# Optimization experiments

Measured on AMD Instinct MI355X. Metric: run time of the kernel, lower is better.

The kernel has to match this reference:

```python
import jax, jax.numpy as jnp
import numpy as np

N_HEADS = 8
N_GROUPS = 32
EPS = 1e-6


def setup_inputs() -> dict:
    key = jax.random.key(0)
    ks = jax.random.split(key, 8)
    b, c, n, K = 2, 512, 1024, 64
    x = jax.random.normal(ks[0], (b, c, n), dtype=jnp.float32)
    valid_mask = jax.random.randint(ks[1], (n, K), 0, 2, dtype=jnp.int32)
    # ensure every query attends to at least one key (avoids all--inf softmax rows)
    valid_mask = valid_mask.at[:, 0].set(1)
    attend_idx = jax.random.randint(ks[2], (n, K), 0, n, dtype=jnp.int64)
    scale = 0.03
    return {
        "x": x,
        "valid_mask": valid_mask,
        "attend_idx": attend_idx,
        "gn_gamma": jnp.ones((c,), jnp.float32),
        "gn_beta": jnp.zeros((c,), jnp.float32),
        "wq": jax.random.normal(ks[3], (c, c), jnp.float32) * scale,
        "bq": jnp.zeros((c,), jnp.float32),
        "wk": jax.random.normal(ks[4], (c, c), jnp.float32) * scale,
        "bk": jnp.zeros((c,), jnp.float32),
        "wv": jax.random.normal(ks[5], (c, c), jnp.float32) * scale,
        "bv": jnp.zeros((c,), jnp.float32),
        "wo": jax.random.normal(ks[6], (c, c), jnp.float32) * scale,
        "bo": jnp.zeros((c,), jnp.float32),
    }


def _group_norm(x, gamma, beta):
    b, c, n = x.shape
    xr = x.reshape(b, N_GROUPS, c // N_GROUPS, n)
    mu = xr.mean(axis=(2, 3), keepdims=True)
    var = xr.var(axis=(2, 3), keepdims=True)
    h = ((xr - mu) * jax.lax.rsqrt(var + EPS)).reshape(b, c, n)
    return h * gamma[None, :, None] + beta[None, :, None]


def reference(x, valid_mask, attend_idx, gn_gamma, gn_beta,
              wq, bq, wk, bk, wv, bv, wo, bo):
    b, c, n = x.shape
    H = N_HEADS
    dh = c // H
    h = _group_norm(x, gn_gamma, gn_beta)
    # 1x1 Conv1d == per-node linear projection
    proj = lambda w, bias: jnp.einsum('oc,bcn->bon', w, h) + bias[None, :, None]
    q = proj(wq, bq).reshape(b, H, dh, n)
    k = proj(wk, bk).reshape(b, H, dh, n)
    v = proj(wv, bv).reshape(b, H, dh, n)
    # gather attendable keys/values per query: [b, H, nq, K, dh]
    kT = jnp.transpose(k, (0, 1, 3, 2))  # [b, H, n, dh]
    vT = jnp.transpose(v, (0, 1, 3, 2))
    keys = jnp.take(kT, attend_idx, axis=2)
    vals = jnp.take(vT, attend_idx, axis=2)
    # NOTE: sparse_forward uses beta=1 (no 1/sqrt(dh) scaling)
    w = jnp.einsum('bhqkc,bhcq->bhqk', keys, q)
    w = jnp.where(valid_mask[None, None] == 0, -jnp.inf, w)
    w = jax.nn.softmax(w, axis=-1)
    o = jnp.einsum('bhqk,bhqkc->bhqc', w, vals)  # [b, H, n, dh]
    # permute(0,3,1,2).reshape(b,c,n): channel layout is (dh, H)
    o = jnp.transpose(o, (0, 3, 1, 2)).reshape(b, c, n)
    out = x + jnp.einsum('oc,bcn->bon', wo, o) + bo[None, :, None]
    return out
```

## Files before the change

### kernel.cpp

```cpp
#include <hip/hip_runtime.h>
#include <hip/hip_bf16.h>

#define B_   2
#define C_   512
#define N_   1024
#define KK_  64
#define H_   8
#define DH_  64
#define NG_  32
#define MQKV 1536

typedef __attribute__((ext_vector_type(8))) short short8;
typedef __attribute__((ext_vector_type(4))) float f32x4;

__device__ __forceinline__ float ldf(const void* p, size_t i, int isbf) {
  return isbf ? __bfloat162float(((const __hip_bfloat16*)p)[i])
              : ((const float*)p)[i];
}
__device__ __forceinline__ unsigned short f2bfu(float f) {
  __hip_bfloat16 h = __float2bfloat16(f);
  unsigned short u; __builtin_memcpy(&u, &h, 2); return u;
}
__device__ __forceinline__ float bfu2f(unsigned short u) {
  return __uint_as_float(((unsigned)u) << 16);
}
__device__ __forceinline__ int detect_bf(const void* gamma) {
  return ((const unsigned*)gamma)[0] == 0x3F803F80u;
}

__global__ __launch_bounds__(256) void conv_k(
    const void* x, const void* wq, const void* wk, const void* wv, const void* wo,
    const void* bq, const void* bk, const void* bv, const void* bo,
    const void* gamma, unsigned short* __restrict__ wqkv,
    unsigned short* __restrict__ wob, float* __restrict__ bqkv,
    float* __restrict__ bof, float2* __restrict__ part) {
  const int isbf = detect_bf(gamma);
  const int tid = threadIdx.x;
  int idx = blockIdx.x * 256 + tid;
  if (idx < MQKV * C_) {
    int m = idx >> 9, c = idx & 511;
    const void* src = (m < 512) ? wq : (m < 1024 ? wk : wv);
    wqkv[idx] = f2bfu(ldf(src, (size_t)(m & 511) * C_ + c, isbf));
  }
  if (idx < C_ * C_) wob[idx] = f2bfu(ldf(wo, idx, isbf));
  if (idx < MQKV) {
    const void* src = (idx < 512) ? bq : (idx < 1024 ? bk : bv);
    bqkv[idx] = ldf(src, idx & 511, isbf);
  }
  if (idx < C_) bof[idx] = ldf(bo, idx, isbf);

  __shared__ float ssum[256], ssq[256];
  if (blockIdx.x < 256) {
    const size_t base = (size_t)blockIdx.x * 4096;
    float sum = 0.f, sq = 0.f;
    if (isbf) {
      const uint4* p = (const uint4*)((const unsigned short*)x + base);
      for (int t = tid; t < 512; t += 256) {
        uint4 u = p[t];
        unsigned wv4[4] = {u.x, u.y, u.z, u.w};
#pragma unroll
        for (int q = 0; q < 4; q++) {
          float a = __uint_as_float(wv4[q] << 16);
          float b = __uint_as_float(wv4[q] & 0xffff0000u);
          sum += a + b; sq += a * a + b * b;
        }
      }
    } else {
      const float4* p = (const float4*)((const float*)x + base);
      for (int t = tid; t < 1024; t += 256) {
        float4 v = p[t];
        sum += v.x + v.y + v.z + v.w;
        sq  += v.x * v.x + v.y * v.y + v.z * v.z + v.w * v.w;
      }
    }
    ssum[tid] = sum; ssq[tid] = sq;
    __syncthreads();
    for (int s = 128; s > 0; s >>= 1) {
      if (tid < s) { ssum[tid] += ssum[tid + s]; ssq[tid] += ssq[tid + s]; }
      __syncthreads();
    }
    if (tid == 0) part[blockIdx.x] = make_float2(ssum[0], ssq[0]);
  }
}

__global__ __launch_bounds__(256) void gn_apply_k(
    const void* x, const void* gamma, const void* beta,
    const float2* __restrict__ part, unsigned short* __restrict__ hT) {
  const int isbf = detect_bf(gamma);
  const int n0 = blockIdx.x * 64, c0 = blockIdx.y * 64, b = blockIdx.z;
  const int tid = threadIdx.x;
  __shared__ unsigned short Lt[64][72];
#pragma unroll
  for (int p = 0; p < 2; p++) {
    int idx = tid + p * 256;
    int cl = idx >> 3, seg = idx & 7;
    int c = c0 + cl;
    int bgi = (b * NG_ + (c >> 4)) * 4;
    float2 p0 = part[bgi], p1 = part[bgi + 1], p2 = part[bgi + 2], p3 = part[bgi + 3];
    float S = p0.x + p1.x + p2.x + p3.x;
    float Q = p0.y + p1.y + p2.y + p3.y;
    float mu = S * (1.f / 16384.f);
    float rs = rsqrtf(fmaxf(Q * (1.f / 16384.f) - mu * mu, 0.f) + 1e-6f);
    float ga = ldf(gamma, c, isbf), be = ldf(beta, c, isbf);
    size_t srow = ((size_t)b * C_ + c) * N_ + n0 + seg * 8;
    float v[8];
    if (isbf) {
      uint4 u = *(const uint4*)((const unsigned short*)x + srow);
      v[0] = __uint_as_float(u.x << 16); v[1] = __uint_as_float(u.x & 0xffff0000u);
      v[2] = __uint_as_float(u.y << 16); v[3] = __uint_as_float(u.y & 0xffff0000u);
      v[4] = __uint_as_float(u.z << 16); v[5] = __uint_as_float(u.z & 0xffff0000u);
      v[6] = __uint_as_float(u.w << 16); v[7] = __uint_as_float(u.w & 0xffff0000u);
    } else {
      float4 a = *(const float4*)((const float*)x + srow);
      float4 bb = *(const float4*)((const float*)x + srow + 4);
      v[0] = a.x; v[1] = a.y; v[2] = a.z; v[3] = a.w;
      v[4] = bb.x; v[5] = bb.y; v[6] = bb.z; v[7] = bb.w;
    }
#pragma unroll
    for (int e = 0; e < 8; e++)
      Lt[seg * 8 + e][cl] = f2bfu((v[e] - mu) * rs * ga + be);
  }
  __syncthreads();
#pragma unroll
  for (int p = 0; p < 2; p++) {
    int idx = tid + p * 256;
    int nl = idx >> 3, seg = idx & 7;
    uint4 v = *(const uint4*)&Lt[nl][seg * 8];
    *(uint4*)&hT[((size_t)b * N_ + n0 + nl) * C_ + c0 + seg * 8] = v;
  }
}

__global__ __launch_bounds__(256) void qkv_gemm_k(
    const unsigned short* __restrict__ wqkv, const unsigned short* __restrict__ hT,
    const float* __restrict__ bqkv, unsigned short* __restrict__ qkv) {
  __shared__ short As[4096], Bs[4096];
  const int tid = threadIdx.x;
  const int lane = tid & 63, wave = tid >> 6;
  const int wm = wave >> 1, wn = wave & 1;
  const int n0 = blockIdx.x * 128;
  const int m0 = blockIdx.y * 128;
  const int b  = blockIdx.z;
  const unsigned short* Bbase = hT + (size_t)b * N_ * C_;

  f32x4 acc[4][4];
#pragma unroll
  for (int i = 0; i < 4; i++)
#pragma unroll
    for (int j = 0; j < 4; j++) acc[i][j] = (f32x4){0.f, 0.f, 0.f, 0.f};

  for (int k0 = 0; k0 < C_; k0 += 32) {
    __syncthreads();
#pragma unroll
    for (int p = 0; p < 2; p++) {
      int i = tid + p * 256;
      int sub = i >> 6, l = i & 63;
      int r = l & 15, kh = (l >> 4) << 3;
      *(uint4*)&As[i * 8] =
          *(const uint4*)&wqkv[(size_t)(m0 + sub * 16 + r) * C_ + k0 + kh];
      *(uint4*)&Bs[i * 8] =
          *(const uint4*)&Bbase[(size_t)(n0 + sub * 16 + r) * C_ + k0 + kh];
    }
    __syncthreads();
    const short8* Av = (const short8*)As;
    const short8* Bv = (const short8*)Bs;
    short8 af[4], bg[4];
#pragma unroll
    for (int i = 0; i < 4; i++) af[i] = Av[(wm * 4 + i) * 64 + lane];
#pragma unroll
    for (int j = 0; j < 4; j++) bg[j] = Bv[(wn * 4 + j) * 64 + lane];
#pragma unroll
    for (int i = 0; i < 4; i++)
#pragma unroll
      for (int j = 0; j < 4; j++)
        acc[i][j] = __builtin_amdgcn_mfma_f32_16x16x32_bf16(af[i], bg[j], acc[i][j], 0, 0, 0);
  }

  const int mb = m0 + wm * 64;
#pragma unroll
  for (int i = 0; i < 4; i++) {
    int mrow0 = mb + i * 16 + ((lane >> 4) << 2);
    int mat = mrow0 >> 9, head = (mrow0 >> 6) & 7, d0 = mrow0 & 63;
    float b0 = bqkv[mrow0], b1 = bqkv[mrow0 + 1], b2 = bqkv[mrow0 + 2], b3 = bqkv[mrow0 + 3];
#pragma unroll
    for (int j = 0; j < 4; j++) {
      int n = n0 + wn * 64 + j * 16 + (lane & 15);
      uint2 st;
      st.x = (unsigned)f2bfu(acc[i][j][0] + b0) | ((unsigned)f2bfu(acc[i][j][1] + b1) << 16);
      st.y = (unsigned)f2bfu(acc[i][j][2] + b2) | ((unsigned)f2bfu(acc[i][j][3] + b3) << 16);
      size_t dst = (size_t)mat * ((size_t)B_ * H_ * N_ * DH_) +
                   (((size_t)b * H_ + head) * N_ + n) * DH_ + d0;
      *(uint2*)&qkv[dst] = st;
    }
  }
}

__global__ __launch_bounds__(512) void attn_k(
    const unsigned short* __restrict__ qkv, const void* aidx,
    const int* __restrict__ vmask, unsigned short* __restrict__ ocT) {
  const int tid = threadIdx.x, w = tid >> 6, lane = tid & 63;
  const int b = blockIdx.x >> 10, qi = blockIdx.x & 1023;

  const unsigned* aw = (const unsigned*)aidx;
  unsigned long long bal = __ballot(aw[2 * lane + 1] != 0u);
  const int is64 = (bal == 0ull);

  __shared__ float qs[8][64];
  __shared__ float wl[8][64];
  __shared__ int   il[8][64];
  __shared__ unsigned short olds[512];

  const size_t S = (size_t)B_ * H_ * N_ * DH_;
  const unsigned short* qT = qkv;
  const unsigned short* kT = qkv + S;
  const unsigned short* vT = qkv + 2 * S;
  const size_t bh = ((size_t)b * H_ + w) * N_;

  qs[w][lane] = bfu2f(qT[(bh + qi) * DH_ + lane]);
  const size_t ai = (size_t)qi * KK_ + lane;
  int idx = is64 ? (int)((const long long*)aidx)[ai] : ((const int*)aidx)[ai];
  idx &= (N_ - 1);
  const int valid = vmask[ai];
  __threadfence_block();

  const uint4* k4 = (const uint4*)&kT[(bh + idx) * DH_];
  float s = 0.f;
#pragma unroll
  for (int j2 = 0; j2 < 8; j2++) {
    uint4 u = k4[j2];
    const float* q8 = &qs[w][j2 * 8];
    s += __uint_as_float(u.x << 16) * q8[0] + __uint_as_float(u.x & 0xffff0000u) * q8[1]
       + __uint_as_float(u.y << 16) * q8[2] + __uint_as_float(u.y & 0xffff0000u) * q8[3]
       + __uint_as_float(u.z << 16) * q8[4] + __uint_as_float(u.z & 0xffff0000u) * q8[5]
       + __uint_as_float(u.w << 16) * q8[6] + __uint_as_float(u.w & 0xffff0000u) * q8[7];
  }
  s = valid ? s : -INFINITY;

  float m = s;
#pragma unroll
  for (int off = 32; off > 0; off >>= 1) m = fmaxf(m, __shfl_xor(m, off));
  float e = valid ? __expf(s - m) : 0.f;
  float sum = e;
#pragma unroll
  for (int off = 32; off > 0; off >>= 1) sum += __shfl_xor(sum, off);

  wl[w][lane] = (sum > 0.f) ? (e / sum) : 0.f;
  il[w][lane] = idx;
  __threadfence_block();

  const unsigned short* vbase = vT + bh * DH_;
  float acc = 0.f;
#pragma unroll 16
  for (int ki = 0; ki < KK_; ki++)
    acc += wl[w][ki] * bfu2f(vbase[(size_t)il[w][ki] * DH_ + lane]);

  olds[lane * H_ + w] = f2bfu(acc);
  __syncthreads();
  if (tid < 64) {
    uint4 vv = *(const uint4*)&olds[tid * 8];
    *(uint4*)&ocT[((size_t)b * N_ + qi) * C_ + tid * 8] = vv;
  }
}

__global__ __launch_bounds__(256) void out_gemm_k(
    const unsigned short* __restrict__ wob, const unsigned short* __restrict__ ocT,
    const float* __restrict__ bof, const void* __restrict__ x,
    const void* gamma, void* __restrict__ out) {
  const int isbf = detect_bf(gamma);
  __shared__ short As[4096], Bs[4096];
  const int tid = threadIdx.x;
  const int lane = tid & 63, wave = tid >> 6;
  const int wm = wave >> 1, wn = wave & 1;
  const int n0 = blockIdx.x * 128;
  const int m0 = blockIdx.y * 128;
  const int b  = blockIdx.z;
  const unsigned short* Bbase = ocT + (size_t)b * N_ * C_;

  f32x4 acc[4][4];
#pragma unroll
  for (int i = 0; i < 4; i++)
#pragma unroll
    for (int j = 0; j < 4; j++) acc[i][j] = (f32x4){0.f, 0.f, 0.f, 0.f};

  for (int k0 = 0; k0 < C_; k0 += 32) {
    __syncthreads();
#pragma unroll
    for (int p = 0; p < 2; p++) {
      int i = tid + p * 256;
      int sub = i >> 6, l = i & 63;
      int r = l & 15, kh = (l >> 4) << 3;
      *(uint4*)&As[i * 8] =
          *(const uint4*)&wob[(size_t)(m0 + sub * 16 + r) * C_ + k0 + kh];
      *(uint4*)&Bs[i * 8] =
          *(const uint4*)&Bbase[(size_t)(n0 + sub * 16 + r) * C_ + k0 + kh];
    }
    __syncthreads();
    const short8* Av = (const short8*)As;
    const short8* Bv = (const short8*)Bs;
    short8 af[4], bg[4];
#pragma unroll
    for (int i = 0; i < 4; i++) af[i] = Av[(wm * 4 + i) * 64 + lane];
#pragma unroll
    for (int j = 0; j < 4; j++) bg[j] = Bv[(wn * 4 + j) * 64 + lane];
#pragma unroll
    for (int i = 0; i < 4; i++)
#pragma unroll
      for (int j = 0; j < 4; j++)
        acc[i][j] = __builtin_amdgcn_mfma_f32_16x16x32_bf16(bg[j], af[i], acc[i][j], 0, 0, 0);
  }

#pragma unroll
  for (int i = 0; i < 4; i++) {
    int m = m0 + wm * 64 + i * 16 + (lane & 15);
    float bias = bof[m];
#pragma unroll
    for (int j = 0; j < 4; j++) {
      int nb = n0 + wn * 64 + j * 16 + ((lane >> 4) << 2);
      size_t oi = ((size_t)b * C_ + m) * N_ + nb;
      if (isbf) {
        const unsigned short* xp = (const unsigned short*)x;
        uint2 xv = *(const uint2*)&xp[oi];
        uint2 st;
        st.x = (unsigned)f2bfu(bfu2f((unsigned short)(xv.x & 0xffff)) + acc[i][j][0] + bias) |
               ((unsigned)f2bfu(bfu2f((unsigned short)(xv.x >> 16)) + acc[i][j][1] + bias) << 16);
        st.y = (unsigned)f2bfu(bfu2f((unsigned short)(xv.y & 0xffff)) + acc[i][j][2] + bias) |
               ((unsigned)f2bfu(bfu2f((unsigned short)(xv.y >> 16)) + acc[i][j][3] + bias) << 16);
        *(uint2*)&((unsigned short*)out)[oi] = st;
      } else {
        const float* xp = (const float*)x;
        float4 xv = *(const float4*)&xp[oi];
        float4 st;
        st.x = xv.x + acc[i][j][0] + bias;
        st.y = xv.y + acc[i][j][1] + bias;
        st.z = xv.z + acc[i][j][2] + bias;
        st.w = xv.w + acc[i][j][3] + bias;
        *(float4*)&((float*)out)[oi] = st;
      }
    }
  }
}

extern "C" void kernel_launch(void* const* d_in, const int* in_sizes, int n_in,
                              void* d_out, int out_size, void* d_ws, size_t ws_size,
                              hipStream_t stream) {
  const void* x     = d_in[0];
  const int*  vmask = (const int*)d_in[1];
  const void* aidx  = d_in[2];
  const void* gamma = d_in[3];
  const void* beta  = d_in[4];
  const void* wq = d_in[5],  *bq = d_in[6];
  const void* wk = d_in[7],  *bk = d_in[8];
  const void* wv = d_in[9],  *bv = d_in[10];
  const void* wo = d_in[11], *bo = d_in[12];

  char* wsb = (char*)d_ws;
  float2* part = (float2*)wsb;
  float*  bqkv = (float*)(wsb + 4096);
  float*  bof  = (float*)(wsb + 12288);
  unsigned short* wqkv = (unsigned short*)(wsb + 16384);
  unsigned short* wob  = wqkv + (size_t)MQKV * C_;
  unsigned short* hT   = wob + (size_t)C_ * C_;
  unsigned short* qkv  = hT + (size_t)B_ * N_ * C_;
  unsigned short* ocT  = qkv + (size_t)3 * B_ * H_ * N_ * DH_;

  conv_k<<<(MQKV * C_) / 256, 256, 0, stream>>>(x, wq, wk, wv, wo, bq, bk, bv, bo,
                                                gamma, wqkv, wob, bqkv, bof, part);
  gn_apply_k<<<dim3(N_ / 64, C_ / 64, B_), 256, 0, stream>>>(x, gamma, beta, part, hT);
  qkv_gemm_k<<<dim3(N_ / 128, MQKV / 128, B_), 256, 0, stream>>>(wqkv, hT, bqkv, qkv);
  attn_k<<<B_ * N_, 512, 0, stream>>>(qkv, aidx, vmask, ocT);
  out_gemm_k<<<dim3(N_ / 128, C_ / 128, B_), 256, 0, stream>>>(wob, ocT, bof, x, gamma, d_out);
}
```

Measured before the change: 156.1 us.

## Fuse weight conversion and group-norm apply into GEMM loads with double buffering

Drops the separate weight-conversion and group-norm-apply kernels. The GEMMs now read fp32 weights and raw x directly, converting to bf16 on the fly and applying a precomputed per-channel scale and shift from a small finalize kernel. Both GEMMs gain register prefetch with double-buffered shared memory so global loads overlap the MFMA work. The cost is that weights are converted redundantly in every block, and the x loads in the QKV GEMM become strided scalar reads along the channel axis, which are less coalesced.

```diff
diff --git a/kernel.cpp b/kernel.cpp
--- a/kernel.cpp
+++ b/kernel.cpp
@@ -8,7 +8,6 @@
 #define H_   8
 #define DH_  64
 #define NG_  32
-#define MQKV 1536
 
 typedef __attribute__((ext_vector_type(8))) short short8;
 typedef __attribute__((ext_vector_type(4))) float f32x4;
@@ -28,119 +27,106 @@
   return ((const unsigned*)gamma)[0] == 0x3F803F80u;
 }
 
-__global__ __launch_bounds__(256) void conv_k(
-    const void* x, const void* wq, const void* wk, const void* wv, const void* wo,
-    const void* bq, const void* bk, const void* bv, const void* bo,
-    const void* gamma, unsigned short* __restrict__ wqkv,
-    unsigned short* __restrict__ wob, float* __restrict__ bqkv,
-    float* __restrict__ bof, float2* __restrict__ part) {
+__global__ __launch_bounds__(256) void stats_k(
+    const void* x, const void* gamma, float2* __restrict__ part) {
   const int isbf = detect_bf(gamma);
   const int tid = threadIdx.x;
-  int idx = blockIdx.x * 256 + tid;
-  if (idx < MQKV * C_) {
-    int m = idx >> 9, c = idx & 511;
-    const void* src = (m < 512) ? wq : (m < 1024 ? wk : wv);
-    wqkv[idx] = f2bfu(ldf(src, (size_t)(m & 511) * C_ + c, isbf));
-  }
-  if (idx < C_ * C_) wob[idx] = f2bfu(ldf(wo, idx, isbf));
-  if (idx < MQKV) {
-    const void* src = (idx < 512) ? bq : (idx < 1024 ? bk : bv);
-    bqkv[idx] = ldf(src, idx & 511, isbf);
-  }
-  if (idx < C_) bof[idx] = ldf(bo, idx, isbf);
-
+  const size_t base = (size_t)blockIdx.x * 4096;
   __shared__ float ssum[256], ssq[256];
-  if (blockIdx.x < 256) {
-    const size_t base = (size_t)blockIdx.x * 4096;
-    float sum = 0.f, sq = 0.f;
-    if (isbf) {
-      const uint4* p = (const uint4*)((const unsigned short*)x + base);
-      for (int t = tid; t < 512; t += 256) {
-        uint4 u = p[t];
-        unsigned wv4[4] = {u.x, u.y, u.z, u.w};
-#pragma unroll
-        for (int q = 0; q < 4; q++) {
-          float a = __uint_as_float(wv4[q] << 16);
-          float b = __uint_as_float(wv4[q] & 0xffff0000u);
-          sum += a + b; sq += a * a + b * b;
-        }
+  float sum = 0.f, sq = 0.f;
+  if (isbf) {
+    const uint4* p = (const uint4*)((const unsigned short*)x + base);
+    for (int t = tid; t < 512; t += 256) {
+      uint4 u = p[t];
+      unsigned wv4[4] = {u.x, u.y, u.z, u.w};
+#pragma unroll
+      for (int q = 0; q < 4; q++) {
+        float a = __uint_as_float(wv4[q] << 16);
+        float b = __uint_as_float(wv4[q] & 0xffff0000u);
+        sum += a + b; sq += a * a + b * b;
       }
-    } else {
-      const float4* p = (const float4*)((const float*)x + base);
-      for (int t = tid; t < 1024; t += 256) {
-        float4 v = p[t];
-        sum += v.x + v.y + v.z + v.w;
-        sq  += v.x * v.x + v.y * v.y + v.z * v.z + v.w * v.w;
-      }
-    }
-    ssum[tid] = sum; ssq[tid] = sq;
+    }
+  } else {
+    const float4* p = (const float4*)((const float*)x + base);
+    for (int t = tid; t < 1024; t += 256) {
+      float4 v = p[t];
+      sum += v.x + v.y + v.z + v.w;
+      sq  += v.x * v.x + v.y * v.y + v.z * v.z + v.w * v.w;
+    }
+  }
+  ssum[tid] = sum; ssq[tid] = sq;
+  __syncthreads();
+  for (int s = 128; s > 0; s >>= 1) {
+    if (tid < s) { ssum[tid] += ssum[tid + s]; ssq[tid] += ssq[tid + s]; }
     __syncthreads();
-    for (int s = 128; s > 0; s >>= 1) {
-      if (tid < s) { ssum[tid] += ssum[tid + s]; ssq[tid] += ssq[tid + s]; }
-      __syncthreads();
-    }
-    if (tid == 0) part[blockIdx.x] = make_float2(ssum[0], ssq[0]);
-  }
-}
-
-__global__ __launch_bounds__(256) void gn_apply_k(
-    const void* x, const void* gamma, const void* beta,
-    const float2* __restrict__ part, unsigned short* __restrict__ hT) {
+  }
+  if (tid == 0) part[blockIdx.x] = make_float2(ssum[0], ssq[0]);
+}
+
+__global__ __launch_bounds__(256) void fin_k(
+    const void* gamma, const void* beta,
+    const void* bq, const void* bk, const void* bv, const void* bo2,
+    const float2* __restrict__ part, float* __restrict__ ab,
+    float* __restrict__ bqkv, float* __restrict__ bof) {
   const int isbf = detect_bf(gamma);
-  const int n0 = blockIdx.x * 64, c0 = blockIdx.y * 64, b = blockIdx.z;
-  const int tid = threadIdx.x;
-  __shared__ unsigned short Lt[64][72];
-#pragma unroll
-  for (int p = 0; p < 2; p++) {
-    int idx = tid + p * 256;
-    int cl = idx >> 3, seg = idx & 7;
-    int c = c0 + cl;
-    int bgi = (b * NG_ + (c >> 4)) * 4;
-    float2 p0 = part[bgi], p1 = part[bgi + 1], p2 = part[bgi + 2], p3 = part[bgi + 3];
+  const int j = blockIdx.x, t = threadIdx.x;
+  if (j < 4) {
+    int b = t & 1, c = j * 128 + (t >> 1);
+    int bg = (b * NG_ + (c >> 4)) * 4;
+    float2 p0 = part[bg], p1 = part[bg + 1], p2 = part[bg + 2], p3 = part[bg + 3];
     float S = p0.x + p1.x + p2.x + p3.x;
     float Q = p0.y + p1.y + p2.y + p3.y;
     float mu = S * (1.f / 16384.f);
     float rs = rsqrtf(fmaxf(Q * (1.f / 16384.f) - mu * mu, 0.f) + 1e-6f);
-    float ga = ldf(gamma, c, isbf), be = ldf(beta, c, isbf);
-    size_t srow = ((size_t)b * C_ + c) * N_ + n0 + seg * 8;
-    float v[8];
-    if (isbf) {
-      uint4 u = *(const uint4*)((const unsigned short*)x + srow);
-      v[0] = __uint_as_float(u.x << 16); v[1] = __uint_as_float(u.x & 0xffff0000u);
-      v[2] = __uint_as_float(u.y << 16); v[3] = __uint_as_float(u.y & 0xffff0000u);
-      v[4] = __uint_as_float(u.z << 16); v[5] = __uint_as_float(u.z & 0xffff0000u);
-      v[6] = __uint_as_float(u.w << 16); v[7] = __uint_as_float(u.w & 0xffff0000u);
-    } else {
-      float4 a = *(const float4*)((const float*)x + srow);
-      float4 bb = *(const float4*)((const float*)x + srow + 4);
-      v[0] = a.x; v[1] = a.y; v[2] = a.z; v[3] = a.w;
-      v[4] = bb.x; v[5] = bb.y; v[6] = bb.z; v[7] = bb.w;
-    }
-#pragma unroll
-    for (int e = 0; e < 8; e++)
-      Lt[seg * 8 + e][cl] = f2bfu((v[e] - mu) * rs * ga + be);
-  }
-  __syncthreads();
-#pragma unroll
-  for (int p = 0; p < 2; p++) {
-    int idx = tid + p * 256;
-    int nl = idx >> 3, seg = idx & 7;
-    uint4 v = *(const uint4*)&Lt[nl][seg * 8];
-    *(uint4*)&hT[((size_t)b * N_ + n0 + nl) * C_ + c0 + seg * 8] = v;
+    float a = rs * ldf(gamma, c, isbf);
+    ab[((size_t)b * C_ + c) * 2]     = a;
+    ab[((size_t)b * C_ + c) * 2 + 1] = ldf(beta, c, isbf) - mu * a;
+  } else if (j < 7) {
+    int base = (j - 4) * 512;
+    for (int t2 = t; t2 < 512; t2 += 256) {
+      int idx = base + t2;
+      const void* src = idx < 512 ? bq : (idx < 1024 ? bk : bv);
+      bqkv[idx] = ldf(src, idx & 511, isbf);
+    }
+  } else {
+    for (int t2 = t; t2 < 512; t2 += 256) bof[t2] = ldf(bo2, t2, isbf);
   }
 }
 
 __global__ __launch_bounds__(256) void qkv_gemm_k(
-    const unsigned short* __restrict__ wqkv, const unsigned short* __restrict__ hT,
-    const float* __restrict__ bqkv, unsigned short* __restrict__ qkv) {
-  __shared__ short As[4096], Bs[4096];
+    const void* wq, const void* wk, const void* wv, const void* gamma,
+    const void* x, const float* __restrict__ ab, const float* __restrict__ bqkv,
+    unsigned short* __restrict__ qkv) {
+  const int isbf = detect_bf(gamma);
+  __shared__ short As[2][4096], Bs[2][4096];
+  __shared__ float abl[512][2];
   const int tid = threadIdx.x;
   const int lane = tid & 63, wave = tid >> 6;
   const int wm = wave >> 1, wn = wave & 1;
   const int n0 = blockIdx.x * 128;
   const int m0 = blockIdx.y * 128;
   const int b  = blockIdx.z;
-  const unsigned short* Bbase = hT + (size_t)b * N_ * C_;
+  const int mat = m0 >> 9, mloc = m0 & 511;
+  const void* wsel = mat == 0 ? wq : (mat == 1 ? wk : wv);
+
+  {
+    const float2* src = (const float2*)ab + (size_t)b * C_;
+    float2 v0 = src[tid], v1 = src[tid + 256];
+    abl[tid][0] = v0.x;       abl[tid][1] = v0.y;
+    abl[tid + 256][0] = v1.x; abl[tid + 256][1] = v1.y;
+  }
+  __syncthreads();
+
+  int sidx[2], aoff[2], bch[2];
+  size_t boff[2];
+#pragma unroll
+  for (int p = 0; p < 2; p++) {
+    int i = tid + p * 256, sub = i >> 6, l = i & 63, r = l & 15, g = l >> 4;
+    sidx[p] = i * 8;
+    aoff[p] = (mloc + sub * 16 + r) * C_ + g * 8;
+    bch[p]  = g * 8;
+    boff[p] = ((size_t)b * C_ + g * 8) * N_ + (n0 + sub * 16 + r);
+  }
 
   f32x4 acc[4][4];
 #pragma unroll
@@ -148,38 +134,66 @@
 #pragma unroll
     for (int j = 0; j < 4; j++) acc[i][j] = (f32x4){0.f, 0.f, 0.f, 0.f};
 
-  for (int k0 = 0; k0 < C_; k0 += 32) {
+  uint4 aR[2]; unsigned short bR[2][8];
+
+#define QKV_PREFETCH(K0)                                                        \
+  _Pragma("unroll") for (int p = 0; p < 2; p++) {                               \
+    if (isbf) {                                                                 \
+      aR[p] = *(const uint4*)((const unsigned short*)wsel + aoff[p] + (K0));    \
+      const unsigned short* xp =                                                \
+          (const unsigned short*)x + boff[p] + (size_t)(K0) * N_;               \
+      _Pragma("unroll") for (int e = 0; e < 8; e++) bR[p][e] = xp[e * N_];      \
+    } else {                                                                    \
+      const float* wf = (const float*)wsel + aoff[p] + (K0);                    \
+      float4 f0 = *(const float4*)wf, f1 = *(const float4*)(wf + 4);            \
+      aR[p].x = (unsigned)f2bfu(f0.x) | ((unsigned)f2bfu(f0.y) << 16);          \
+      aR[p].y = (unsigned)f2bfu(f0.z) | ((unsigned)f2bfu(f0.w) << 16);          \
+      aR[p].z = (unsigned)f2bfu(f1.x) | ((unsigned)f2bfu(f1.y) << 16);          \
+      aR[p].w = (unsigned)f2bfu(f1.z) | ((unsigned)f2bfu(f1.w) << 16);          \
+      const float* xf = (const float*)x + boff[p] + (size_t)(K0) * N_;          \
+      _Pragma("unroll") for (int e = 0; e < 8; e++) bR[p][e] = f2bfu(xf[e * N_]); \
+    }                                                                           \
+  }
+
+  QKV_PREFETCH(0)
+  for (int kt = 0; kt < 16; kt++) {
+    const int buf = kt & 1, k0 = kt * 32;
+#pragma unroll
+    for (int p = 0; p < 2; p++) {
+      *(uint4*)&As[buf][sidx[p]] = aR[p];
+      unsigned pk[4];
+#pragma unroll
+      for (int e2 = 0; e2 < 4; e2++) {
+        int c0 = k0 + bch[p] + e2 * 2;
+        float v0 = fmaf(abl[c0][0],     bfu2f(bR[p][e2 * 2]),     abl[c0][1]);
+        float v1 = fmaf(abl[c0 + 1][0], bfu2f(bR[p][e2 * 2 + 1]), abl[c0 + 1][1]);
+        pk[e2] = (unsigned)f2bfu(v0) | ((unsigned)f2bfu(v1) << 16);
+      }
+      uint4 bv4; bv4.x = pk[0]; bv4.y = pk[1]; bv4.z = pk[2]; bv4.w = pk[3];
+      *(uint4*)&Bs[buf][sidx[p]] = bv4;
+    }
     __syncthreads();
-#pragma unroll
-    for (int p = 0; p < 2; p++) {
-      int i = tid + p * 256;
-      int sub = i >> 6, l = i & 63;
-      int r = l & 15, kh = (l >> 4) << 3;
-      *(uint4*)&As[i * 8] =
-          *(const uint4*)&wqkv[(size_t)(m0 + sub * 16 + r) * C_ + k0 + kh];
-      *(uint4*)&Bs[i * 8] =
-          *(const uint4*)&Bbase[(size_t)(n0 + sub * 16 + r) * C_ + k0 + kh];
-    }
-    __syncthreads();
-    const short8* Av = (const short8*)As;
-    const short8* Bv = (const short8*)Bs;
-    short8 af[4], bg[4];
+    if (kt < 15) { QKV_PREFETCH(k0 + 32) }
+    const short8* Av = (const short8*)As[buf];
+    const short8* Bv = (const short8*)Bs[buf];
+    short8 af[4], bg4[4];
 #pragma unroll
     for (int i = 0; i < 4; i++) af[i] = Av[(wm * 4 + i) * 64 + lane];
 #pragma unroll
-    for (int j = 0; j < 4; j++) bg[j] = Bv[(wn * 4 + j) * 64 + lane];
+    for (int j = 0; j < 4; j++) bg4[j] = Bv[(wn * 4 + j) * 64 + lane];
 #pragma unroll
     for (int i = 0; i < 4; i++)
 #pragma unroll
       for (int j = 0; j < 4; j++)
-        acc[i][j] = __builtin_amdgcn_mfma_f32_16x16x32_bf16(af[i], bg[j], acc[i][j], 0, 0, 0);
-  }
+        acc[i][j] = __builtin_amdgcn_mfma_f32_16x16x32_bf16(af[i], bg4[j], acc[i][j], 0, 0, 0);
+  }
+#undef QKV_PREFETCH
 
   const int mb = m0 + wm * 64;
 #pragma unroll
   for (int i = 0; i < 4; i++) {
     int mrow0 = mb + i * 16 + ((lane >> 4) << 2);
-    int mat = mrow0 >> 9, head = (mrow0 >> 6) & 7, d0 = mrow0 & 63;
+    int mat2 = mrow0 >> 9, head = (mrow0 >> 6) & 7, d0 = mrow0 & 63;
     float b0 = bqkv[mrow0], b1 = bqkv[mrow0 + 1], b2 = bqkv[mrow0 + 2], b3 = bqkv[mrow0 + 3];
 #pragma unroll
     for (int j = 0; j < 4; j++) {
@@ -187,7 +201,7 @@
       uint2 st;
       st.x = (unsigned)f2bfu(acc[i][j][0] + b0) | ((unsigned)f2bfu(acc[i][j][1] + b1) << 16);
       st.y = (unsigned)f2bfu(acc[i][j][2] + b2) | ((unsigned)f2bfu(acc[i][j][3] + b3) << 16);
-      size_t dst = (size_t)mat * ((size_t)B_ * H_ * N_ * DH_) +
+      size_t dst = (size_t)mat2 * ((size_t)B_ * H_ * N_ * DH_) +
                    (((size_t)b * H_ + head) * N_ + n) * DH_ + d0;
       *(uint2*)&qkv[dst] = st;
     }
@@ -262,11 +276,11 @@
 }
 
 __global__ __launch_bounds__(256) void out_gemm_k(
-    const unsigned short* __restrict__ wob, const unsigned short* __restrict__ ocT,
+    const void* wo, const unsigned short* __restrict__ ocT,
     const float* __restrict__ bof, const void* __restrict__ x,
     const void* gamma, void* __restrict__ out) {
   const int isbf = detect_bf(gamma);
-  __shared__ short As[4096], Bs[4096];
+  __shared__ short As[2][4096], Bs[2][4096];
   const int tid = threadIdx.x;
   const int lane = tid & 63, wave = tid >> 6;
   const int wm = wave >> 1, wn = wave & 1;
@@ -275,38 +289,62 @@
   const int b  = blockIdx.z;
   const unsigned short* Bbase = ocT + (size_t)b * N_ * C_;
 
+  int sidx[2], aoff[2], boff[2];
+#pragma unroll
+  for (int p = 0; p < 2; p++) {
+    int i = tid + p * 256, sub = i >> 6, l = i & 63, r = l & 15, g = l >> 4;
+    sidx[p] = i * 8;
+    aoff[p] = (m0 + sub * 16 + r) * C_ + g * 8;
+    boff[p] = (n0 + sub * 16 + r) * C_ + g * 8;
+  }
+
   f32x4 acc[4][4];
 #pragma unroll
   for (int i = 0; i < 4; i++)
 #pragma unroll
     for (int j = 0; j < 4; j++) acc[i][j] = (f32x4){0.f, 0.f, 0.f, 0.f};
 
-  for (int k0 = 0; k0 < C_; k0 += 32) {
+  uint4 aR[2], bRv[2];
+
+#define OUT_PREFETCH(K0)                                                        \
+  _Pragma("unroll") for (int p = 0; p < 2; p++) {                               \
+    if (isbf) {                                                                 \
+      aR[p] = *(const uint4*)((const unsigned short*)wo + aoff[p] + (K0));      \
+    } else {                                                                    \
+      const float* wf = (const float*)wo + aoff[p] + (K0);                      \
+      float4 f0 = *(const float4*)wf, f1 = *(const float4*)(wf + 4);            \
+      aR[p].x = (unsigned)f2bfu(f0.x) | ((unsigned)f2bfu(f0.y) << 16);          \
+      aR[p].y = (unsigned)f2bfu(f0.z) | ((unsigned)f2bfu(f0.w) << 16);          \
+      aR[p].z = (unsigned)f2bfu(f1.x) | ((unsigned)f2bfu(f1.y) << 16);          \
+      aR[p].w = (unsigned)f2bfu(f1.z) | ((unsigned)f2bfu(f1.w) << 16);          \
+    }                                                                           \
+    bRv[p] = *(const uint4*)(Bbase + boff[p] + (K0));                           \
+  }
+
+  OUT_PREFETCH(0)
+  for (int kt = 0; kt < 16; kt++) {
+    const int buf = kt & 1, k0 = kt * 32;
+#pragma unroll
+    for (int p = 0; p < 2; p++) {
+      *(uint4*)&As[buf][sidx[p]] = aR[p];
+      *(uint4*)&Bs[buf][sidx[p]] = bRv[p];
+    }
     __syncthreads();
-#pragma unroll
-    for (int p = 0; p < 2; p++) {
-      int i = tid + p * 256;
-      int sub = i >> 6, l = i & 63;
-      int r = l & 15, kh = (l >> 4) << 3;
-      *(uint4*)&As[i * 8] =
-          *(const uint4*)&wob[(size_t)(m0 + sub * 16 + r) * C_ + k0 + kh];
-      *(uint4*)&Bs[i * 8] =
-          *(const uint4*)&Bbase[(size_t)(n0 + sub * 16 + r) * C_ + k0 + kh];
-    }
-    __syncthreads();
-    const short8* Av = (const short8*)As;
-    const short8* Bv = (const short8*)Bs;
-    short8 af[4], bg[4];
+    if (kt < 15) { OUT_PREFETCH(k0 + 32) }
+    const short8* Av = (const short8*)As[buf];
+    const short8* Bv = (const short8*)Bs[buf];
+    short8 af[4], bg4[4];
 #pragma unroll
     for (int i = 0; i < 4; i++) af[i] = Av[(wm * 4 + i) * 64 + lane];
 #pragma unroll
-    for (int j = 0; j < 4; j++) bg[j] = Bv[(wn * 4 + j) * 64 + lane];
+    for (int j = 0; j < 4; j++) bg4[j] = Bv[(wn * 4 + j) * 64 + lane];
 #pragma unroll
     for (int i = 0; i < 4; i++)
 #pragma unroll
       for (int j = 0; j < 4; j++)
-        acc[i][j] = __builtin_amdgcn_mfma_f32_16x16x32_bf16(bg[j], af[i], acc[i][j], 0, 0, 0);
-  }
+        acc[i][j] = __builtin_amdgcn_mfma_f32_16x16x32_bf16(bg4[j], af[i], acc[i][j], 0, 0, 0);
+  }
+#undef OUT_PREFETCH
 
 #pragma unroll
   for (int i = 0; i < 4; i++) {
@@ -354,18 +392,17 @@
 
   char* wsb = (char*)d_ws;
   float2* part = (float2*)wsb;
-  float*  bqkv = (float*)(wsb + 4096);
-  float*  bof  = (float*)(wsb + 12288);
-  unsigned short* wqkv = (unsigned short*)(wsb + 16384);
-  unsigned short* wob  = wqkv + (size_t)MQKV * C_;
-  unsigned short* hT   = wob + (size_t)C_ * C_;
-  unsigned short* qkv  = hT + (size_t)B_ * N_ * C_;
-  unsigned short* ocT  = qkv + (size_t)3 * B_ * H_ * N_ * DH_;
-
-  conv_k<<<(MQKV * C_) / 256, 256, 0, stream>>>(x, wq, wk, wv, wo, bq, bk, bv, bo,
-                                                gamma, wqkv, wob, bqkv, bof, part);
-  gn_apply_k<<<dim3(N_ / 64, C_ / 64, B_), 256, 0, stream>>>(x, gamma, beta, part, hT);
-  qkv_gemm_k<<<dim3(N_ / 128, MQKV / 128, B_), 256, 0, stream>>>(wqkv, hT, bqkv, qkv);
+  float*  ab   = (float*)(wsb + 4096);
+  float*  bqkv = (float*)(wsb + 16384);
+  float*  bof  = (float*)(wsb + 24576);
+  unsigned short* qkv = (unsigned short*)(wsb + 32768);
+  unsigned short* ocT = qkv + (size_t)3 * B_ * H_ * N_ * DH_;
+
+  stats_k<<<256, 256, 0, stream>>>(x, gamma, part);
+  fin_k<<<8, 256, 0, stream>>>(gamma, beta, bq, bk, bv, bo, part, ab, bqkv, bof);
+  qkv_gemm_k<<<dim3(N_ / 128, 1536 / 128, B_), 256, 0, stream>>>(
+      wq, wk, wv, gamma, x, ab, bqkv, qkv);
   attn_k<<<B_ * N_, 512, 0, stream>>>(qkv, aidx, vmask, ocT);
-  out_gemm_k<<<dim3(N_ / 128, C_ / 128, B_), 256, 0, stream>>>(wob, ocT, bof, x, gamma, d_out);
-}
+  out_gemm_k<<<dim3(N_ / 128, C_ / 128, B_), 256, 0, stream>>>(
+      wo, ocT, bof, x, gamma, d_out);
+}
```

Measured after the change: 187.8 us. +20.4%, slower.

## Fuse weight bf16 conversion into GEMM loads and double-buffer smaller GEMM tiles

Applied to the files above, without the earlier changes.

Drops the separate weight-conversion pass and turns the old conv kernel into a stats-only kernel. Both GEMMs now read fp32 weights directly and convert them to bf16 while loading them into registers. The GEMMs move to 64x128 tiles, which doubles the block count, and use register prefetch into double-buffered shared memory so the next tile's loads overlap the MFMA work on the current one. GroupNorm apply is folded into a single fma per element. The cost is that every GEMM block re-converts the weights on each call, and fp32 weight reads use twice the bandwidth of bf16.

```diff
diff --git a/kernel.cpp b/kernel.cpp
--- a/kernel.cpp
+++ b/kernel.cpp
@@ -8,7 +8,6 @@
 #define H_   8
 #define DH_  64
 #define NG_  32
-#define MQKV 1536
 
 typedef __attribute__((ext_vector_type(8))) short short8;
 typedef __attribute__((ext_vector_type(4))) float f32x4;
@@ -28,59 +27,40 @@
   return ((const unsigned*)gamma)[0] == 0x3F803F80u;
 }
 
-__global__ __launch_bounds__(256) void conv_k(
-    const void* x, const void* wq, const void* wk, const void* wv, const void* wo,
-    const void* bq, const void* bk, const void* bv, const void* bo,
-    const void* gamma, unsigned short* __restrict__ wqkv,
-    unsigned short* __restrict__ wob, float* __restrict__ bqkv,
-    float* __restrict__ bof, float2* __restrict__ part) {
+__global__ __launch_bounds__(256) void stats_k(
+    const void* x, const void* gamma, float2* __restrict__ part) {
   const int isbf = detect_bf(gamma);
   const int tid = threadIdx.x;
-  int idx = blockIdx.x * 256 + tid;
-  if (idx < MQKV * C_) {
-    int m = idx >> 9, c = idx & 511;
-    const void* src = (m < 512) ? wq : (m < 1024 ? wk : wv);
-    wqkv[idx] = f2bfu(ldf(src, (size_t)(m & 511) * C_ + c, isbf));
-  }
-  if (idx < C_ * C_) wob[idx] = f2bfu(ldf(wo, idx, isbf));
-  if (idx < MQKV) {
-    const void* src = (idx < 512) ? bq : (idx < 1024 ? bk : bv);
-    bqkv[idx] = ldf(src, idx & 511, isbf);
-  }
-  if (idx < C_) bof[idx] = ldf(bo, idx, isbf);
-
+  const size_t base = (size_t)blockIdx.x * 4096;
   __shared__ float ssum[256], ssq[256];
-  if (blockIdx.x < 256) {
-    const size_t base = (size_t)blockIdx.x * 4096;
-    float sum = 0.f, sq = 0.f;
-    if (isbf) {
-      const uint4* p = (const uint4*)((const unsigned short*)x + base);
-      for (int t = tid; t < 512; t += 256) {
-        uint4 u = p[t];
-        unsigned wv4[4] = {u.x, u.y, u.z, u.w};
-#pragma unroll
-        for (int q = 0; q < 4; q++) {
-          float a = __uint_as_float(wv4[q] << 16);
-          float b = __uint_as_float(wv4[q] & 0xffff0000u);
-          sum += a + b; sq += a * a + b * b;
-        }
-      }
-    } else {
-      const float4* p = (const float4*)((const float*)x + base);
-      for (int t = tid; t < 1024; t += 256) {
-        float4 v = p[t];
-        sum += v.x + v.y + v.z + v.w;
-        sq  += v.x * v.x + v.y * v.y + v.z * v.z + v.w * v.w;
+  float sum = 0.f, sq = 0.f;
+  if (isbf) {
+    const uint4* p = (const uint4*)((const unsigned short*)x + base);
+    for (int t = tid; t < 512; t += 256) {
+      uint4 u = p[t];
+      unsigned wv4[4] = {u.x, u.y, u.z, u.w};
+#pragma unroll
+      for (int q = 0; q < 4; q++) {
+        float a = __uint_as_float(wv4[q] << 16);
+        float b = __uint_as_float(wv4[q] & 0xffff0000u);
+        sum += a + b; sq += a * a + b * b;
       }
     }
-    ssum[tid] = sum; ssq[tid] = sq;
+  } else {
+    const float4* p = (const float4*)((const float*)x + base);
+    for (int t = tid; t < 1024; t += 256) {
+      float4 v = p[t];
+      sum += v.x + v.y + v.z + v.w;
+      sq  += v.x * v.x + v.y * v.y + v.z * v.z + v.w * v.w;
+    }
+  }
+  ssum[tid] = sum; ssq[tid] = sq;
+  __syncthreads();
+  for (int s = 128; s > 0; s >>= 1) {
+    if (tid < s) { ssum[tid] += ssum[tid + s]; ssq[tid] += ssq[tid + s]; }
     __syncthreads();
-    for (int s = 128; s > 0; s >>= 1) {
-      if (tid < s) { ssum[tid] += ssum[tid + s]; ssq[tid] += ssq[tid + s]; }
-      __syncthreads();
-    }
-    if (tid == 0) part[blockIdx.x] = make_float2(ssum[0], ssq[0]);
-  }
+  }
+  if (tid == 0) part[blockIdx.x] = make_float2(ssum[0], ssq[0]);
 }
 
 __global__ __launch_bounds__(256) void gn_apply_k(
@@ -101,7 +81,8 @@
     float Q = p0.y + p1.y + p2.y + p3.y;
     float mu = S * (1.f / 16384.f);
     float rs = rsqrtf(fmaxf(Q * (1.f / 16384.f) - mu * mu, 0.f) + 1e-6f);
-    float ga = ldf(gamma, c, isbf), be = ldf(beta, c, isbf);
+    float ga = rs * ldf(gamma, c, isbf);
+    float be = ldf(beta, c, isbf) - mu * ga;
     size_t srow = ((size_t)b * C_ + c) * N_ + n0 + seg * 8;
     float v[8];
     if (isbf) {
@@ -118,7 +99,7 @@
     }
 #pragma unroll
     for (int e = 0; e < 8; e++)
-      Lt[seg * 8 + e][cl] = f2bfu((v[e] - mu) * rs * ga + be);
+      Lt[seg * 8 + e][cl] = f2bfu(fmaf(v[e], ga, be));
   }
   __syncthreads();
 #pragma unroll
@@ -131,56 +112,86 @@
 }
 
 __global__ __launch_bounds__(256) void qkv_gemm_k(
-    const unsigned short* __restrict__ wqkv, const unsigned short* __restrict__ hT,
-    const float* __restrict__ bqkv, unsigned short* __restrict__ qkv) {
-  __shared__ short As[4096], Bs[4096];
+    const void* wq, const void* wk, const void* wv,
+    const void* bq, const void* bk, const void* bv, const void* gamma,
+    const unsigned short* __restrict__ hT, unsigned short* __restrict__ qkv) {
+  const int isbf = detect_bf(gamma);
+  __shared__ short As[2][2048], Bs[2][4096];
   const int tid = threadIdx.x;
   const int lane = tid & 63, wave = tid >> 6;
   const int wm = wave >> 1, wn = wave & 1;
   const int n0 = blockIdx.x * 128;
-  const int m0 = blockIdx.y * 128;
+  const int mg0 = blockIdx.y * 64;
   const int b  = blockIdx.z;
-  const unsigned short* Bbase = hT + (size_t)b * N_ * C_;
-
-  f32x4 acc[4][4];
-#pragma unroll
-  for (int i = 0; i < 4; i++)
+  const int mat = mg0 >> 9, mloc = mg0 & 511;
+  const void* wsel = mat == 0 ? wq : (mat == 1 ? wk : wv);
+  const void* bsel = mat == 0 ? bq : (mat == 1 ? bk : bv);
+
+  const int asub = tid >> 6, al = tid & 63, ar = al & 15, ag = al >> 4;
+  const int a_sidx = tid * 8;
+  const int aoff = (mloc + asub * 16 + ar) * C_ + ag * 8;
+  int b_sidx[2]; size_t boff[2];
+#pragma unroll
+  for (int p = 0; p < 2; p++) {
+    int i = tid + p * 256, sub = i >> 6, l = i & 63, r = l & 15, g = l >> 4;
+    b_sidx[p] = i * 8;
+    boff[p] = ((size_t)b * N_ + n0 + sub * 16 + r) * C_ + g * 8;
+  }
+
+  f32x4 acc[2][4];
+#pragma unroll
+  for (int i = 0; i < 2; i++)
 #pragma unroll
     for (int j = 0; j < 4; j++) acc[i][j] = (f32x4){0.f, 0.f, 0.f, 0.f};
 
-  for (int k0 = 0; k0 < C_; k0 += 32) {
+  uint4 aR, bRv[2];
+
+#define QKV_PREFETCH(K0)                                                        \
+  {                                                                             \
+    if (isbf) {                                                                 \
+      aR = *(const uint4*)((const unsigned short*)wsel + aoff + (K0));          \
+    } else {                                                                    \
+      const float* wf = (const float*)wsel + aoff + (K0);                       \
+      float4 f0 = *(const float4*)wf, f1 = *(const float4*)(wf + 4);            \
+      aR.x = (unsigned)f2bfu(f0.x) | ((unsigned)f2bfu(f0.y) << 16);             \
+      aR.y = (unsigned)f2bfu(f0.z) | ((unsigned)f2bfu(f0.w) << 16);             \
+      aR.z = (unsigned)f2bfu(f1.x) | ((unsigned)f2bfu(f1.y) << 16);             \
+      aR.w = (unsigned)f2bfu(f1.z) | ((unsigned)f2bfu(f1.w) << 16);             \
+    }                                                                           \
+    _Pragma("unroll") for (int p = 0; p < 2; p++)                               \
+      bRv[p] = *(const uint4*)(hT + boff[p] + (K0));                            \
+  }
+
+  QKV_PREFETCH(0)
+  for (int kt = 0; kt < 16; kt++) {
+    const int buf = kt & 1, k0 = kt * 32;
+    *(uint4*)&As[buf][a_sidx] = aR;
+#pragma unroll
+    for (int p = 0; p < 2; p++) *(uint4*)&Bs[buf][b_sidx[p]] = bRv[p];
     __syncthreads();
-#pragma unroll
-    for (int p = 0; p < 2; p++) {
-      int i = tid + p * 256;
-      int sub = i >> 6, l = i & 63;
-      int r = l & 15, kh = (l >> 4) << 3;
-      *(uint4*)&As[i * 8] =
-          *(const uint4*)&wqkv[(size_t)(m0 + sub * 16 + r) * C_ + k0 + kh];
-      *(uint4*)&Bs[i * 8] =
-          *(const uint4*)&Bbase[(size_t)(n0 + sub * 16 + r) * C_ + k0 + kh];
-    }
-    __syncthreads();
-    const short8* Av = (const short8*)As;
-    const short8* Bv = (const short8*)Bs;
-    short8 af[4], bg[4];
-#pragma unroll
-    for (int i = 0; i < 4; i++) af[i] = Av[(wm * 4 + i) * 64 + lane];
-#pragma unroll
-    for (int j = 0; j < 4; j++) bg[j] = Bv[(wn * 4 + j) * 64 + lane];
-#pragma unroll
-    for (int i = 0; i < 4; i++)
+    if (kt < 15) { QKV_PREFETCH(k0 + 32) }
+    const short8* Av = (const short8*)As[buf];
+    const short8* Bv = (const short8*)Bs[buf];
+    short8 af[2], bg4[4];
+#pragma unroll
+    for (int i = 0; i < 2; i++) af[i] = Av[(wm * 2 + i) * 64 + lane];
+#pragma unroll
+    for (int j = 0; j < 4; j++) bg4[j] = Bv[(wn * 4 + j) * 64 + lane];
+#pragma unroll
+    for (int i = 0; i < 2; i++)
 #pragma unroll
       for (int j = 0; j < 4; j++)
-        acc[i][j] = __builtin_amdgcn_mfma_f32_16x16x32_bf16(af[i], bg[j], acc[i][j], 0, 0, 0);
-  }
-
-  const int mb = m0 + wm * 64;
-#pragma unroll
-  for (int i = 0; i < 4; i++) {
-    int mrow0 = mb + i * 16 + ((lane >> 4) << 2);
-    int mat = mrow0 >> 9, head = (mrow0 >> 6) & 7, d0 = mrow0 & 63;
-    float b0 = bqkv[mrow0], b1 = bqkv[mrow0 + 1], b2 = bqkv[mrow0 + 2], b3 = bqkv[mrow0 + 3];
+        acc[i][j] = __builtin_amdgcn_mfma_f32_16x16x32_bf16(af[i], bg4[j], acc[i][j], 0, 0, 0);
+  }
+#undef QKV_PREFETCH
+
+#pragma unroll
+  for (int i = 0; i < 2; i++) {
+    int mrow0 = mg0 + wm * 32 + i * 16 + ((lane >> 4) << 2);
+    int o = mrow0 & 511;
+    int head = o >> 6, d0 = o & 63;
+    float b0 = ldf(bsel, o, isbf),     b1 = ldf(bsel, o + 1, isbf);
+    float b2 = ldf(bsel, o + 2, isbf), b3 = ldf(bsel, o + 3, isbf);
 #pragma unroll
     for (int j = 0; j < 4; j++) {
       int n = n0 + wn * 64 + j * 16 + (lane & 15);
@@ -262,56 +273,80 @@
 }
 
 __global__ __launch_bounds__(256) void out_gemm_k(
-    const unsigned short* __restrict__ wob, const unsigned short* __restrict__ ocT,
-    const float* __restrict__ bof, const void* __restrict__ x,
-    const void* gamma, void* __restrict__ out) {
+    const void* wo, const void* bo2, const unsigned short* __restrict__ ocT,
+    const void* __restrict__ x, const void* gamma, void* __restrict__ out) {
   const int isbf = detect_bf(gamma);
-  __shared__ short As[4096], Bs[4096];
+  __shared__ short As[2][2048], Bs[2][4096];
   const int tid = threadIdx.x;
   const int lane = tid & 63, wave = tid >> 6;
   const int wm = wave >> 1, wn = wave & 1;
   const int n0 = blockIdx.x * 128;
-  const int m0 = blockIdx.y * 128;
+  const int m0 = blockIdx.y * 64;
   const int b  = blockIdx.z;
   const unsigned short* Bbase = ocT + (size_t)b * N_ * C_;
 
-  f32x4 acc[4][4];
-#pragma unroll
-  for (int i = 0; i < 4; i++)
+  const int asub = tid >> 6, al = tid & 63, ar = al & 15, ag = al >> 4;
+  const int a_sidx = tid * 8;
+  const int aoff = (m0 + asub * 16 + ar) * C_ + ag * 8;
+  int b_sidx[2], boff[2];
+#pragma unroll
+  for (int p = 0; p < 2; p++) {
+    int i = tid + p * 256, sub = i >> 6, l = i & 63, r = l & 15, g = l >> 4;
+    b_sidx[p] = i * 8;
+    boff[p] = (n0 + sub * 16 + r) * C_ + g * 8;
+  }
+
+  f32x4 acc[2][4];
+#pragma unroll
+  for (int i = 0; i < 2; i++)
 #pragma unroll
     for (int j = 0; j < 4; j++) acc[i][j] = (f32x4){0.f, 0.f, 0.f, 0.f};
 
-  for (int k0 = 0; k0 < C_; k0 += 32) {
+  uint4 aR, bRv[2];
+
+#define OUT_PREFETCH(K0)                                                        \
+  {                                                                             \
+    if (isbf) {                                                                 \
+      aR = *(const uint4*)((const unsigned short*)wo + aoff + (K0));            \
+    } else {                                                                    \
+      const float* wf = (const float*)wo + aoff + (K0);                         \
+      float4 f0 = *(const float4*)wf, f1 = *(const float4*)(wf + 4);            \
+      aR.x = (unsigned)f2bfu(f0.x) | ((unsigned)f2bfu(f0.y) << 16);             \
+      aR.y = (unsigned)f2bfu(f0.z) | ((unsigned)f2bfu(f0.w) << 16);             \
+      aR.z = (unsigned)f2bfu(f1.x) | ((unsigned)f2bfu(f1.y) << 16);             \
+      aR.w = (unsigned)f2bfu(f1.z) | ((unsigned)f2bfu(f1.w) << 16);             \
+    }                                                                           \
+    _Pragma("unroll") for (int p = 0; p < 2; p++)                               \
+      bRv[p] = *(const uint4*)(Bbase + boff[p] + (K0));                         \
+  }
+
+  OUT_PREFETCH(0)
+  for (int kt = 0; kt < 16; kt++) {
+    const int buf = kt & 1, k0 = kt * 32;
+    *(uint4*)&As[buf][a_sidx] = aR;
+#pragma unroll
+    for (int p = 0; p < 2; p++) *(uint4*)&Bs[buf][b_sidx[p]] = bRv[p];
     __syncthreads();
-#pragma unroll
-    for (int p = 0; p < 2; p++) {
-      int i = tid + p * 256;
-      int sub = i >> 6, l = i & 63;
-      int r = l & 15, kh = (l >> 4) << 3;
-      *(uint4*)&As[i * 8] =
-          *(const uint4*)&wob[(size_t)(m0 + sub * 16 + r) * C_ + k0 + kh];
-      *(uint4*)&Bs[i * 8] =
-          *(const uint4*)&Bbase[(size_t)(n0 + sub * 16 + r) * C_ + k0 + kh];
-    }
-    __syncthreads();
-    const short8* Av = (const short8*)As;
-    const short8* Bv = (const short8*)Bs;
-    short8 af[4], bg[4];
-#pragma unroll
-    for (int i = 0; i < 4; i++) af[i] = Av[(wm * 4 + i) * 64 + lane];
-#pragma unroll
-    for (int j = 0; j < 4; j++) bg[j] = Bv[(wn * 4 + j) * 64 + lane];
-#pragma unroll
-    for (int i = 0; i < 4; i++)
+    if (kt < 15) { OUT_PREFETCH(k0 + 32) }
+    const short8* Av = (const short8*)As[buf];
+    const short8* Bv = (const short8*)Bs[buf];
+    short8 af[2], bg4[4];
+#pragma unroll
+    for (int i = 0; i < 2; i++) af[i] = Av[(wm * 2 + i) * 64 + lane];
+#pragma unroll
+    for (int j = 0; j < 4; j++) bg4[j] = Bv[(wn * 4 + j) * 64 + lane];
+#pragma unroll
+    for (int i = 0; i < 2; i++)
 #pragma unroll
       for (int j = 0; j < 4; j++)
-        acc[i][j] = __builtin_amdgcn_mfma_f32_16x16x32_bf16(bg[j], af[i], acc[i][j], 0, 0, 0);
-  }
-
-#pragma unroll
-  for (int i = 0; i < 4; i++) {
-    int m = m0 + wm * 64 + i * 16 + (lane & 15);
-    float bias = bof[m];
+        acc[i][j] = __builtin_amdgcn_mfma_f32_16x16x32_bf16(bg4[j], af[i], acc[i][j], 0, 0, 0);
+  }
+#undef OUT_PREFETCH
+
+#pragma unroll
+  for (int i = 0; i < 2; i++) {
+    int m = m0 + wm * 32 + i * 16 + (lane & 15);
+    float bias = ldf(bo2, m, isbf);
 #pragma unroll
     for (int j = 0; j < 4; j++) {
       int nb = n0 + wn * 64 + j * 16 + ((lane >> 4) << 2);
@@ -354,18 +389,15 @@
 
   char* wsb = (char*)d_ws;
   float2* part = (float2*)wsb;
-  float*  bqkv = (float*)(wsb + 4096);
-  float*  bof  = (float*)(wsb + 12288);
-  unsigned short* wqkv = (unsigned short*)(wsb + 16384);
-  unsigned short* wob  = wqkv + (size_t)MQKV * C_;
-  unsigned short* hT   = wob + (size_t)C_ * C_;
-  unsigned short* qkv  = hT + (size_t)B_ * N_ * C_;
-  unsigned short* ocT  = qkv + (size_t)3 * B_ * H_ * N_ * DH_;
-
-  conv_k<<<(MQKV * C_) / 256, 256, 0, stream>>>(x, wq, wk, wv, wo, bq, bk, bv, bo,
-                                                gamma, wqkv, wob, bqkv, bof, part);
+  unsigned short* hT  = (unsigned short*)(wsb + 4096);
+  unsigned short* qkv = hT + (size_t)B_ * N_ * C_;
+  unsigned short* ocT = qkv + (size_t)3 * B_ * H_ * N_ * DH_;
+
+  stats_k<<<256, 256, 0, stream>>>(x, gamma, part);
   gn_apply_k<<<dim3(N_ / 64, C_ / 64, B_), 256, 0, stream>>>(x, gamma, beta, part, hT);
-  qkv_gemm_k<<<dim3(N_ / 128, MQKV / 128, B_), 256, 0, stream>>>(wqkv, hT, bqkv, qkv);
+  qkv_gemm_k<<<dim3(N_ / 128, 1536 / 64, B_), 256, 0, stream>>>(
+      wq, wk, wv, bq, bk, bv, gamma, hT, qkv);
   attn_k<<<B_ * N_, 512, 0, stream>>>(qkv, aidx, vmask, ocT);
-  out_gemm_k<<<dim3(N_ / 128, C_ / 128, B_), 256, 0, stream>>>(wob, ocT, bof, x, gamma, d_out);
-}
+  out_gemm_k<<<dim3(N_ / 128, C_ / 64, B_), 256, 0, stream>>>(
+      wo, bo, ocT, x, gamma, d_out);
+}
```

Measured after the change: 160.4 us. 1.03x slower.
